# Kernel optimization log

Measured on AMD Instinct MI355X. Metric: run time of the kernel, lower is better.

## Reference

```python
import jax, jax.numpy as jnp
import numpy as np

B, D_IN, D_OUT, H, DEPTH = 16384, 512, 64, 256, 3
LR, ITERS, EPS = 0.1, 50, 1e-5


def setup_inputs() -> dict:
    key = jax.random.key(0)
    ks = jax.random.split(key, 8)
    d = {}
    d["x"] = jax.random.normal(ks[0], (B, D_IN), jnp.float32)
    d["y0"] = jax.random.normal(ks[1], (B, D_OUT), jnp.float32)
    cur = D_IN + D_OUT
    for i in range(DEPTH):
        d[f"W{i}"] = jax.random.normal(ks[2 + i], (H, cur), jnp.float32) / np.sqrt(cur).astype(np.float32)
        d[f"b{i}"] = jnp.zeros((H,), jnp.float32)
        d[f"g{i}"] = jnp.ones((H,), jnp.float32)
        d[f"be{i}"] = jnp.zeros((H,), jnp.float32)
        cur = H
    d["Wout"] = jax.random.normal(ks[5], (1, H), jnp.float32) / np.sqrt(H).astype(np.float32)
    d["bout"] = jnp.zeros((1,), jnp.float32)
    return d


def _energy(x, y, layers, out_layer):
    # E(x, y): concat -> [Linear -> LayerNorm -> SiLU] * depth -> Linear(1)
    h = jnp.concatenate([x, y], axis=-1)  # [B, D_IN+D_OUT]
    for (W, b, g, be) in layers:
        h = h @ W.T + b  # [B, H]
        mu = jnp.mean(h, axis=-1, keepdims=True)
        var = jnp.var(h, axis=-1, keepdims=True)  # biased, matching torch LayerNorm
        h = (h - mu) * jax.lax.rsqrt(var + EPS) * g + be
        h = h * jax.nn.sigmoid(h)  # SiLU
    Wout, bout = out_layer
    return h @ Wout.T + bout  # [B, 1]


def reference(x, y0, W0, b0, g0, be0, W1, b1, g1, be1, W2, b2, g2, be2, Wout, bout):
    layers = [(W0, b0, g0, be0), (W1, b1, g1, be1), (W2, b2, g2, be2)]
    out_layer = (Wout, bout)

    def e_mean(y):
        return jnp.mean(_energy(x, y, layers, out_layer))

    def step(y, _):
        # SGD on y: y <- y - lr * grad_y E_mean
        return y - LR * jax.grad(e_mean)(y), None

    y_final, _ = jax.lax.scan(step, y0, None, length=ITERS)
    return y_final
```

## Files before the change

### kernel.cpp

```cpp
#include <hip/hip_runtime.h>


typedef unsigned short u16;
typedef u16 u16x4 __attribute__((ext_vector_type(4)));
typedef u16 u16x8 __attribute__((ext_vector_type(8)));
typedef float f32x4 __attribute__((ext_vector_type(4)));
typedef int i32x4 __attribute__((ext_vector_type(4)));
typedef __bf16 bf16x8 __attribute__((ext_vector_type(8)));

#define ITERS 50
#define EPSF 1e-5f
static constexpr float SCALE = 0.1f / 16384.0f;

#define OFF_W0X   0
#define OFF_W0Y   262144
#define OFF_W0YT  278528
#define OFF_W1    294912
#define OFF_W1T   360448
#define OFF_W2    425984
#define OFF_W2T   491520
#define OFF_WSC   557056

__device__ __forceinline__ float bf2f(u16 h) {
  union { unsigned int u; float f; } v; v.u = ((unsigned int)h) << 16; return v.f;
}
__device__ __forceinline__ u16 f2bf(float f) {
  union { float f; unsigned int u; } v; v.f = f;
  unsigned int u = v.u;
  return (u16)((u + 0x7FFFu + ((u >> 16) & 1u)) >> 16);
}
__device__ __forceinline__ f32x4 mfma16(u16x8 a, u16x8 b, f32x4 c) {
  return __builtin_amdgcn_mfma_f32_16x16x32_bf16(
      __builtin_bit_cast(bf16x8, a), __builtin_bit_cast(bf16x8, b), c, 0, 0, 0);
}
__device__ __forceinline__ i32x4 mfma8(i32x4 a, i32x4 b, i32x4 c) {
  return __builtin_amdgcn_mfma_i32_16x16x64_i8(a, b, c, 0, 0, 0);
}
__device__ __forceinline__ int qpack4(const float* v, float qs) {
  int r = 0;
#pragma unroll
  for (int e = 0; e < 4; ++e) {
    float c = fmaxf(-127.f, fminf(127.f, v[e] * qs));
    int xi = __float2int_rn(c);
    r |= (xi & 255) << (8 * e);
  }
  return r;
}

__global__ void prep_w0x(const float* __restrict__ W0, u16* __restrict__ dst) {
  int i = blockIdx.x * 256 + threadIdx.x;
  if (i < 131072) dst[i] = f2bf(W0[(i >> 9) * 576 + (i & 511)]);
}

__global__ void prep_quant(const float* __restrict__ W0, const float* __restrict__ W1,
                           const float* __restrict__ W2, char* __restrict__ ws) {
  int wid = blockIdx.x * 4 + (threadIdx.x >> 6);
  int lane = threadIdx.x & 63;
  float* sc = (float*)(ws + OFF_WSC);
  if (wid < 256) {
    float v = W0[wid * 576 + 512 + lane];
    float mx = fabsf(v);
#pragma unroll
    for (int m = 1; m < 64; m <<= 1) mx = fmaxf(mx, __shfl_xor(mx, m));
    float qs = mx > 0.f ? 127.f / mx : 0.f;
    float c = fmaxf(-127.f, fminf(127.f, v * qs));
    ws[OFF_W0Y + wid * 64 + lane] = (char)__float2int_rn(c);
    if (lane == 0) sc[wid] = mx * (1.f / 127.f);
    return;
  }
  float v[4];
  char* dst;
  if (wid < 320) {
    int r = wid - 256;
#pragma unroll
    for (int e = 0; e < 4; ++e) v[e] = W0[(4 * lane + e) * 576 + 512 + r];
    dst = ws + OFF_W0YT + r * 256;
  } else if (wid < 576) {
    int r = wid - 320;
#pragma unroll
    for (int e = 0; e < 4; ++e) v[e] = W1[r * 256 + 4 * lane + e];
    dst = ws + OFF_W1 + r * 256;
  } else if (wid < 832) {
    int r = wid - 576;
#pragma unroll
    for (int e = 0; e < 4; ++e) v[e] = W1[(4 * lane + e) * 256 + r];
    dst = ws + OFF_W1T + r * 256;
  } else if (wid < 1088) {
    int r = wid - 832;
#pragma unroll
    for (int e = 0; e < 4; ++e) v[e] = W2[r * 256 + 4 * lane + e];
    dst = ws + OFF_W2 + r * 256;
  } else {
    int r = wid - 1088;
#pragma unroll
    for (int e = 0; e < 4; ++e) v[e] = W2[(4 * lane + e) * 256 + r];
    dst = ws + OFF_W2T + r * 256;
  }
  float mx = fmaxf(fmaxf(fabsf(v[0]), fabsf(v[1])), fmaxf(fabsf(v[2]), fabsf(v[3])));
#pragma unroll
  for (int m = 1; m < 64; m <<= 1) mx = fmaxf(mx, __shfl_xor(mx, m));
  float qs = mx > 0.f ? 127.f / mx : 0.f;
  ((int*)dst)[lane] = qpack4(v, qs);
  if (lane == 0) sc[wid] = mx * (1.f / 127.f);
}

template <int KS, int LDB, int AST>
__device__ __forceinline__ void gemm8(const char* A, const char* __restrict__ Bg,
                                      i32x4 (&acc)[2][4], int w, int l15, int q) {
  const char* Ab = A + l15 * AST + q * 16;
  const char* Bb = Bg + (64 * w + l15) * LDB + q * 16;
#pragma unroll
  for (int ks = 0; ks < KS; ++ks) {
    i32x4 b[4];
#pragma unroll
    for (int j = 0; j < 4; ++j) b[j] = *(const i32x4*)(Bb + 16 * j * LDB + ks * 64);
#pragma unroll
    for (int i = 0; i < 2; ++i) {
      i32x4 a = *(const i32x4*)(Ab + 16 * i * AST + ks * 64);
#pragma unroll
      for (int j = 0; j < 4; ++j) acc[i][j] = mfma8(a, b[j], acc[i][j]);
    }
  }
}

__device__ __forceinline__ void gemm_dy8(const char* A, const char* __restrict__ BT,
                                         i32x4 (&dy)[2], int mi, int nb, int l15, int q) {
  const char* Ab = A + (mi * 16 + l15) * 272 + q * 16;
  const char* B0 = BT + (nb + l15) * 256 + q * 16;
  const char* B1 = BT + (nb + 16 + l15) * 256 + q * 16;
#pragma unroll
  for (int ks = 0; ks < 4; ++ks) {
    i32x4 a = *(const i32x4*)(Ab + ks * 64);
    dy[0] = mfma8(a, *(const i32x4*)(B0 + ks * 64), dy[0]);
    dy[1] = mfma8(a, *(const i32x4*)(B1 + ks * 64), dy[1]);
  }
}

__device__ __forceinline__ void epi8(u16* gdst, const i32x4 (&acc)[2][4],
                                     const float* sRow, const float* sCol,
                                     int w, int l15, int q) {
#pragma unroll
  for (int i = 0; i < 2; ++i)
#pragma unroll
    for (int j = 0; j < 4; ++j) {
      int col = 64 * w + 16 * j + l15;
      float sc = sCol[col];
#pragma unroll
      for (int rr = 0; rr < 4; ++rr) {
        int row = 16 * i + 4 * q + rr;
        gdst[row * 264 + col] = f2bf((float)acc[i][j][rr] * sRow[row] * sc);
      }
    }
}

__device__ __forceinline__ void ew_fwd8(const u16* gIn, char* zqOut, float* szh,
                                        char* aOut, float* sAo, const float* bias,
                                        const float* g, const float* be,
                                        float* invOut, int t) {
  const int r = t >> 3, cg = t & 7;
  const u16* zp = gIn + r * 264 + 4 * cg;
  float z[32];
#pragma unroll
  for (int u = 0; u < 8; ++u) {
    u16x4 v = *(const u16x4*)(zp + 32 * u);
#pragma unroll
    for (int e = 0; e < 4; ++e) z[4 * u + e] = bf2f(v[e]);
  }
  if (bias) {
#pragma unroll
    for (int u = 0; u < 8; ++u) {
      f32x4 bv = *(const f32x4*)(bias + 32 * u + 4 * cg);
#pragma unroll
      for (int e = 0; e < 4; ++e) z[4 * u + e] += bv[e];
    }
  }
  float s = 0.f, ss = 0.f;
#pragma unroll
  for (int k = 0; k < 32; ++k) { s += z[k]; ss += z[k] * z[k]; }
  s += __shfl_xor(s, 1); ss += __shfl_xor(ss, 1);
  s += __shfl_xor(s, 2); ss += __shfl_xor(ss, 2);
  s += __shfl_xor(s, 4); ss += __shfl_xor(ss, 4);
  const float mu = s * (1.f / 256.f);
  const float var = ss * (1.f / 256.f) - mu * mu;
  const float inv = rsqrtf(var + EPSF);
  if (cg == 0) invOut[r] = inv;
  float a[32];
  float mzh = 0.f, ma = 0.f;
#pragma unroll
  for (int u = 0; u < 8; ++u) {
    f32x4 gv = *(const f32x4*)(g + 32 * u + 4 * cg);
    f32x4 bev = *(const f32x4*)(be + 32 * u + 4 * cg);
#pragma unroll
    for (int e = 0; e < 4; ++e) {
      const int k = 4 * u + e;
      float zn = (z[k] - mu) * inv;
      z[k] = zn;
      mzh = fmaxf(mzh, fabsf(zn));
      float uu = zn * gv[e] + bev[e];
      float av = uu / (1.f + __expf(-uu));
      a[k] = av;
      ma = fmaxf(ma, fabsf(av));
    }
  }
  mzh = fmaxf(mzh, __shfl_xor(mzh, 1)); ma = fmaxf(ma, __shfl_xor(ma, 1));
  mzh = fmaxf(mzh, __shfl_xor(mzh, 2)); ma = fmaxf(ma, __shfl_xor(ma, 2));
  mzh = fmaxf(mzh, __shfl_xor(mzh, 4)); ma = fmaxf(ma, __shfl_xor(ma, 4));
  float qz = mzh > 0.f ? 127.f / mzh : 0.f;
  float qa = ma > 0.f ? 127.f / ma : 0.f;
  if (cg == 0) { szh[r] = mzh * (1.f / 127.f); sAo[r] = ma * (1.f / 127.f); }
#pragma unroll
  for (int u = 0; u < 8; ++u) {
    *(int*)(zqOut + r * 272 + 32 * u + 4 * cg) = qpack4(&z[4 * u], qz);
    *(int*)(aOut + r * 272 + 32 * u + 4 * cg) = qpack4(&a[4 * u], qa);
  }
}

__device__ __forceinline__ void ew_l2_8(const u16* gIn, char* dOut, float* sAo,
                                        const float* bias, const float* g,
                                        const float* be, const float* wo, int t) {
  const int r = t >> 3, cg = t & 7;
  const u16* zp = gIn + r * 264 + 4 * cg;
  float zh[32], dzh[32];
  float s = 0.f, ss = 0.f;
#pragma unroll
  for (int u = 0; u < 8; ++u) {
    u16x4 v = *(const u16x4*)(zp + 32 * u);
    f32x4 bv = *(const f32x4*)(bias + 32 * u + 4 * cg);
#pragma unroll
    for (int e = 0; e < 4; ++e) {
      float zz = bf2f(v[e]) + bv[e];
      zh[4 * u + e] = zz; s += zz; ss += zz * zz;
    }
  }
  s += __shfl_xor(s, 1); ss += __shfl_xor(ss, 1);
  s += __shfl_xor(s, 2); ss += __shfl_xor(ss, 2);
  s += __shfl_xor(s, 4); ss += __shfl_xor(ss, 4);
  const float mu = s * (1.f / 256.f);
  const float var = ss * (1.f / 256.f) - mu * mu;
  const float inv = rsqrtf(var + EPSF);
  float s1 = 0.f, s2 = 0.f;
#pragma unroll
  for (int u = 0; u < 8; ++u) {
    f32x4 gv = *(const f32x4*)(g + 32 * u + 4 * cg);
    f32x4 bev = *(const f32x4*)(be + 32 * u + 4 * cg);
    f32x4 wv = *(const f32x4*)(wo + 32 * u + 4 * cg);
#pragma unroll
    for (int e = 0; e < 4; ++e) {
      const int k = 4 * u + e;
      float zn = (zh[k] - mu) * inv;
      zh[k] = zn;
      float uu = zn * gv[e] + bev[e];
      float sg = 1.f / (1.f + __expf(-uu));
      float du = wv[e] * sg * (1.f + uu * (1.f - sg));
      float d = du * gv[e];
      dzh[k] = d; s1 += d; s2 += d * zn;
    }
  }
  s1 += __shfl_xor(s1, 1); s2 += __shfl_xor(s2, 1);
  s1 += __shfl_xor(s1, 2); s2 += __shfl_xor(s2, 2);
  s1 += __shfl_xor(s1, 4); s2 += __shfl_xor(s2, 4);
  const float m1 = s1 * (1.f / 256.f), m2 = s2 * (1.f / 256.f);
  float mx = 0.f;
#pragma unroll
  for (int k = 0; k < 32; ++k) {
    dzh[k] = inv * (dzh[k] - m1 - zh[k] * m2);
    mx = fmaxf(mx, fabsf(dzh[k]));
  }
  mx = fmaxf(mx, __shfl_xor(mx, 1));
  mx = fmaxf(mx, __shfl_xor(mx, 2));
  mx = fmaxf(mx, __shfl_xor(mx, 4));
  float qd = mx > 0.f ? 127.f / mx : 0.f;
  if (cg == 0) sAo[r] = mx * (1.f / 127.f);
#pragma unroll
  for (int u = 0; u < 8; ++u)
    *(int*)(dOut + r * 272 + 32 * u + 4 * cg) = qpack4(&dzh[4 * u], qd);
}

__device__ __forceinline__ void ew_bwd8(const u16* gIn, const char* zq, const float* szh,
                                        const float* invArr, const float* g,
                                        const float* be, char* dOut, float* sAo, int t) {
  const int r = t >> 3, cg = t & 7;
  const u16* dp = gIn + r * 264 + 4 * cg;
  const char* zp = zq + r * 272 + 4 * cg;
  const float inv = invArr[r];
  const float szr = szh[r];
  float zh[32], dzh[32];
  float s1 = 0.f, s2 = 0.f;
#pragma unroll
  for (int u = 0; u < 8; ++u) {
    u16x4 dv = *(const u16x4*)(dp + 32 * u);
    int zi = *(const int*)(zp + 32 * u);
    f32x4 gv = *(const f32x4*)(g + 32 * u + 4 * cg);
    f32x4 bev = *(const f32x4*)(be + 32 * u + 4 * cg);
#pragma unroll
    for (int e = 0; e < 4; ++e) {
      const int k = 4 * u + e;
      float zn = (float)((signed char)(zi >> (8 * e))) * szr;
      float da = bf2f(dv[e]);
      float uu = zn * gv[e] + bev[e];
      float sg = 1.f / (1.f + __expf(-uu));
      float du = da * sg * (1.f + uu * (1.f - sg));
      float d = du * gv[e];
      zh[k] = zn; dzh[k] = d; s1 += d; s2 += d * zn;
    }
  }
  s1 += __shfl_xor(s1, 1); s2 += __shfl_xor(s2, 1);
  s1 += __shfl_xor(s1, 2); s2 += __shfl_xor(s2, 2);
  s1 += __shfl_xor(s1, 4); s2 += __shfl_xor(s2, 4);
  const float m1 = s1 * (1.f / 256.f), m2 = s2 * (1.f / 256.f);
  float mx = 0.f;
#pragma unroll
  for (int k = 0; k < 32; ++k) {
    dzh[k] = inv * (dzh[k] - m1 - zh[k] * m2);
    mx = fmaxf(mx, fabsf(dzh[k]));
  }
  mx = fmaxf(mx, __shfl_xor(mx, 1));
  mx = fmaxf(mx, __shfl_xor(mx, 2));
  mx = fmaxf(mx, __shfl_xor(mx, 4));
  float qd = mx > 0.f ? 127.f / mx : 0.f;
  if (cg == 0) sAo[r] = mx * (1.f / 127.f);
#pragma unroll
  for (int u = 0; u < 8; ++u)
    *(int*)(dOut + r * 272 + 32 * u + 4 * cg) = qpack4(&dzh[4 * u], qd);
}

__global__ __launch_bounds__(256, 2) void descent_kernel(
    const float* __restrict__ x, const float* __restrict__ y0,
    const float* __restrict__ b0, const float* __restrict__ g0, const float* __restrict__ be0,
    const float* __restrict__ b1, const float* __restrict__ g1, const float* __restrict__ be1,
    const float* __restrict__ b2, const float* __restrict__ g2, const float* __restrict__ be2,
    const float* __restrict__ wout, const char* __restrict__ ws, float* __restrict__ out) {
  __shared__ __align__(16) char zq0[32 * 272];
  __shared__ __align__(16) char zq1[32 * 272];
  __shared__ __align__(16) char A8[32 * 272];
  __shared__ __align__(16) u16 gT[32 * 264];
  __shared__ __align__(16) char yb[32 * 80];
  __shared__ float params[9 * 256];
  __shared__ float wsc[1344];
  __shared__ float sA[32], szh0[32], szh1[32], sY[32];
  __shared__ float invs[2][32];
  __shared__ float smax[4 * 16];

  const int t = threadIdx.x;
  const int w = t >> 6, lane = t & 63, l15 = lane & 15, q = lane >> 4;
  const int rowbase = blockIdx.x * 32;

  const u16* W0X = (const u16*)(ws + OFF_W0X);
  const char* W0Yq = ws + OFF_W0Y;
  const char* W0YTq = ws + OFF_W0YT;
  const char* W1q = ws + OFF_W1;
  const char* W1Tq = ws + OFF_W1T;
  const char* W2q = ws + OFF_W2;
  const char* W2Tq = ws + OFF_W2T;
  const float* wscg = (const float*)(ws + OFF_WSC);

  params[0 * 256 + t] = g0[t];  params[1 * 256 + t] = be0[t];
  params[2 * 256 + t] = g1[t];  params[3 * 256 + t] = be1[t];
  params[4 * 256 + t] = g2[t];  params[5 * 256 + t] = be2[t];
  params[6 * 256 + t] = b1[t];  params[7 * 256 + t] = b2[t];
  params[8 * 256 + t] = wout[t];
#pragma unroll
  for (int k = 0; k < 6; ++k) {
    int idx = t + 256 * k;
    if (idx < 1344) wsc[idx] = wscg[idx];
  }

  const int mi = w >> 1, nb = (w & 1) * 32;
  float yv[2][4];
#pragma unroll
  for (int j = 0; j < 2; ++j)
#pragma unroll
    for (int rr = 0; rr < 4; ++rr)
      yv[j][rr] = y0[(rowbase + mi * 16 + q * 4 + rr) * 64 + nb + 16 * j + l15];

  const f32x4 z4 = {0.f, 0.f, 0.f, 0.f};

  f32x4 cR[2][4];
#pragma unroll
  for (int i = 0; i < 2; ++i)
#pragma unroll
    for (int j = 0; j < 4; ++j) cR[i][j] = z4;
  {
    const float* xp0 = x + (rowbase + l15) * 512 + q * 8;
    const u16* Bb = W0X + (64 * w + l15) * 512 + q * 8;
#pragma unroll 4
    for (int ks = 0; ks < 16; ++ks) {
      u16x8 b[4];
#pragma unroll
      for (int j = 0; j < 4; ++j) b[j] = *(const u16x8*)(Bb + 16 * j * 512 + ks * 32);
#pragma unroll
      for (int i = 0; i < 2; ++i) {
        const float* xp = xp0 + i * 16 * 512 + ks * 32;
        f32x4 x0 = *(const f32x4*)xp;
        f32x4 x1 = *(const f32x4*)(xp + 4);
        u16x8 a;
#pragma unroll
        for (int e = 0; e < 4; ++e) { a[e] = f2bf(x0[e]); a[4 + e] = f2bf(x1[e]); }
#pragma unroll
        for (int j = 0; j < 4; ++j) cR[i][j] = mfma16(a, b[j], cR[i][j]);
      }
    }
#pragma unroll
    for (int j = 0; j < 4; ++j) {
      float bb = b0[64 * w + 16 * j + l15];
#pragma unroll
      for (int i = 0; i < 2; ++i)
#pragma unroll
        for (int rr = 0; rr < 4; ++rr) cR[i][j][rr] += bb;
    }
  }
  __syncthreads();

  for (int it = 0; it < ITERS; ++it) {
    float mx[4];
#pragma unroll
    for (int rr = 0; rr < 4; ++rr)
      mx[rr] = fmaxf(fabsf(yv[0][rr]), fabsf(yv[1][rr]));
#pragma unroll
    for (int m = 1; m < 16; m <<= 1)
#pragma unroll
      for (int rr = 0; rr < 4; ++rr) mx[rr] = fmaxf(mx[rr], __shfl_xor(mx[rr], m));
    if (l15 == 0)
#pragma unroll
      for (int rr = 0; rr < 4; ++rr) smax[w * 16 + q * 4 + rr] = mx[rr];
    __syncthreads();
#pragma unroll
    for (int rr = 0; rr < 4; ++rr) {
      float m2 = fmaxf(mx[rr], smax[(w ^ 1) * 16 + q * 4 + rr]);
      float qy = m2 > 0.f ? 127.f / m2 : 0.f;
      int row = 16 * mi + 4 * q + rr;
      if (l15 == 0 && (w & 1) == 0) sY[row] = m2 * (1.f / 127.f);
#pragma unroll
      for (int j = 0; j < 2; ++j) {
        float c = fmaxf(-127.f, fminf(127.f, yv[j][rr] * qy));
        yb[row * 80 + nb + 16 * j + l15] = (char)__float2int_rn(c);
      }
    }
    __syncthreads();

    i32x4 acc[2][4];
#pragma unroll
    for (int i = 0; i < 2; ++i)
#pragma unroll
      for (int j = 0; j < 4; ++j) acc[i][j] = (i32x4){0, 0, 0, 0};
    gemm8<1, 64, 80>(yb, W0Yq, acc, w, l15, q);
#pragma unroll
    for (int i = 0; i < 2; ++i)
#pragma unroll
      for (int j = 0; j < 4; ++j) {
        int col = 64 * w + 16 * j + l15;
        float sc = wsc[col];
#pragma unroll
        for (int rr = 0; rr < 4; ++rr) {
          int row = 16 * i + 4 * q + rr;
          gT[row * 264 + col] = f2bf(cR[i][j][rr] + (float)acc[i][j][rr] * sY[row] * sc);
        }
      }
    __syncthreads();
    ew_fwd8(gT, zq0, szh0, A8, sA, nullptr, &params[0 * 256], &params[1 * 256],
            invs[0], t);
    __syncthreads();

#pragma unroll
    for (int i = 0; i < 2; ++i)
#pragma unroll
      for (int j = 0; j < 4; ++j) acc[i][j] = (i32x4){0, 0, 0, 0};
    gemm8<4, 256, 272>(A8, W1q, acc, w, l15, q);
    epi8(gT, acc, sA, &wsc[320], w, l15, q);
    __syncthreads();
    ew_fwd8(gT, zq1, szh1, A8, sA, &params[6 * 256], &params[2 * 256],
            &params[3 * 256], invs[1], t);
    __syncthreads();

#pragma unroll
    for (int i = 0; i < 2; ++i)
#pragma unroll
      for (int j = 0; j < 4; ++j) acc[i][j] = (i32x4){0, 0, 0, 0};
    gemm8<4, 256, 272>(A8, W2q, acc, w, l15, q);
    epi8(gT, acc, sA, &wsc[832], w, l15, q);
    __syncthreads();
    ew_l2_8(gT, A8, sA, &params[7 * 256], &params[4 * 256], &params[5 * 256],
            &params[8 * 256], t);
    __syncthreads();

#pragma unroll
    for (int i = 0; i < 2; ++i)
#pragma unroll
      for (int j = 0; j < 4; ++j) acc[i][j] = (i32x4){0, 0, 0, 0};
    gemm8<4, 256, 272>(A8, W2Tq, acc, w, l15, q);
    epi8(gT, acc, sA, &wsc[1088], w, l15, q);
    __syncthreads();
    ew_bwd8(gT, zq1, szh1, invs[1], &params[2 * 256], &params[3 * 256], A8, sA, t);
    __syncthreads();

#pragma unroll
    for (int i = 0; i < 2; ++i)
#pragma unroll
      for (int j = 0; j < 4; ++j) acc[i][j] = (i32x4){0, 0, 0, 0};
    gemm8<4, 256, 272>(A8, W1Tq, acc, w, l15, q);
    epi8(gT, acc, sA, &wsc[576], w, l15, q);
    __syncthreads();
    ew_bwd8(gT, zq0, szh0, invs[0], &params[0 * 256], &params[1 * 256], A8, sA, t);
    __syncthreads();

    i32x4 dy[2] = {{0, 0, 0, 0}, {0, 0, 0, 0}};
    gemm_dy8(A8, W0YTq, dy, mi, nb, l15, q);
#pragma unroll
    for (int j = 0; j < 2; ++j)
#pragma unroll
      for (int rr = 0; rr < 4; ++rr) {
        int row = 16 * mi + 4 * q + rr;
        yv[j][rr] -= SCALE * (float)dy[j][rr] * sA[row] * wsc[256 + nb + 16 * j + l15];
      }
  }

#pragma unroll
  for (int j = 0; j < 2; ++j)
#pragma unroll
    for (int rr = 0; rr < 4; ++rr)
      out[(rowbase + mi * 16 + q * 4 + rr) * 64 + nb + 16 * j + l15] = yv[j][rr];
}

extern "C" void kernel_launch(void* const* d_in, const int* in_sizes, int n_in,
                              void* d_out, int out_size, void* d_ws, size_t ws_size,
                              hipStream_t stream) {
  const float* x   = (const float*)d_in[0];
  const float* y0  = (const float*)d_in[1];
  const float* W0  = (const float*)d_in[2];
  const float* b0  = (const float*)d_in[3];
  const float* g0  = (const float*)d_in[4];
  const float* be0 = (const float*)d_in[5];
  const float* W1  = (const float*)d_in[6];
  const float* b1  = (const float*)d_in[7];
  const float* g1  = (const float*)d_in[8];
  const float* be1 = (const float*)d_in[9];
  const float* W2  = (const float*)d_in[10];
  const float* b2  = (const float*)d_in[11];
  const float* g2  = (const float*)d_in[12];
  const float* be2 = (const float*)d_in[13];
  const float* wout = (const float*)d_in[14];
  char* ws = (char*)d_ws;
  float* out = (float*)d_out;

  prep_w0x<<<512, 256, 0, stream>>>(W0, (u16*)(ws + OFF_W0X));
  prep_quant<<<336, 256, 0, stream>>>(W0, W1, W2, ws);
  descent_kernel<<<512, 256, 0, stream>>>(x, y0, b0, g0, be0, b1, g1, be1,
                                          b2, g2, be2, wout, ws, out);
}
```

Measured before the change: 2.308 ms.

## Cut shared memory and registers to raise occupancy in int8 descent kernel

Replaces per-row weight quantization scales with per-tensor scales computed by a new absmax kernel. It keeps the saved normalized activations and the LayerNorm inverse-std in registers as packed bf16 instead of int8 shared buffers. It also shrinks the staging buffer, packs the layer-0 residual into bf16 pairs, and raises launch bounds from 2 to 4 blocks per SM. Smaller pieces: truncating bf16 conversion, rcp-based sigmoid, perm-based int8 packing, and bias folded into the GEMM epilogue. The aim is higher occupancy and less shared-memory traffic, at the cost of coarser weight quantization and possible register pressure or spills.

```diff
diff --git a/kernel.cpp b/kernel.cpp
--- a/kernel.cpp
+++ b/kernel.cpp
@@ -2,6 +2,7 @@
 
 
 typedef unsigned short u16;
+typedef u16 u16x2 __attribute__((ext_vector_type(2)));
 typedef u16 u16x4 __attribute__((ext_vector_type(4)));
 typedef u16 u16x8 __attribute__((ext_vector_type(8)));
 typedef float f32x4 __attribute__((ext_vector_type(4)));
@@ -10,6 +11,8 @@
 
 #define ITERS 50
 #define EPSF 1e-5f
+#define STG 262
+#define AST 272
 static constexpr float SCALE = 0.1f / 16384.0f;
 
 #define OFF_W0X   0
@@ -24,10 +27,30 @@
 __device__ __forceinline__ float bf2f(u16 h) {
   union { unsigned int u; float f; } v; v.u = ((unsigned int)h) << 16; return v.f;
 }
+__device__ __forceinline__ u16 f2bt(float f) {
+  return (u16)(__builtin_bit_cast(unsigned int, f) >> 16);
+}
 __device__ __forceinline__ u16 f2bf(float f) {
-  union { float f; unsigned int u; } v; v.f = f;
-  unsigned int u = v.u;
+  unsigned int u = __builtin_bit_cast(unsigned int, f);
   return (u16)((u + 0x7FFFu + ((u >> 16) & 1u)) >> 16);
+}
+__device__ __forceinline__ float uplo(int p) {
+  return __builtin_bit_cast(float, (unsigned int)p << 16);
+}
+__device__ __forceinline__ float uphi(int p) {
+  return __builtin_bit_cast(float, (unsigned int)p & 0xffff0000u);
+}
+__device__ __forceinline__ int packbf2(float lo, float hi) {
+  return __builtin_amdgcn_perm(__builtin_bit_cast(int, hi),
+                               __builtin_bit_cast(int, lo), 0x07060302);
+}
+__device__ __forceinline__ int pack_i8x4(float a0, float a1, float a2, float a3,
+                                         float qs) {
+  int b0 = __float2int_rn(a0 * qs), b1 = __float2int_rn(a1 * qs);
+  int b2 = __float2int_rn(a2 * qs), b3 = __float2int_rn(a3 * qs);
+  int t01 = __builtin_amdgcn_perm(b1, b0, 0x00000400);
+  int t23 = __builtin_amdgcn_perm(b3, b2, 0x00000400);
+  return __builtin_amdgcn_perm(t23, t01, 0x05040100);
 }
 __device__ __forceinline__ f32x4 mfma16(u16x8 a, u16x8 b, f32x4 c) {
   return __builtin_amdgcn_mfma_f32_16x16x32_bf16(
@@ -36,78 +59,72 @@
 __device__ __forceinline__ i32x4 mfma8(i32x4 a, i32x4 b, i32x4 c) {
   return __builtin_amdgcn_mfma_i32_16x16x64_i8(a, b, c, 0, 0, 0);
 }
-__device__ __forceinline__ int qpack4(const float* v, float qs) {
-  int r = 0;
-#pragma unroll
-  for (int e = 0; e < 4; ++e) {
-    float c = fmaxf(-127.f, fminf(127.f, v[e] * qs));
-    int xi = __float2int_rn(c);
-    r |= (xi & 255) << (8 * e);
-  }
-  return r;
-}
 
 __global__ void prep_w0x(const float* __restrict__ W0, u16* __restrict__ dst) {
   int i = blockIdx.x * 256 + threadIdx.x;
   if (i < 131072) dst[i] = f2bf(W0[(i >> 9) * 576 + (i & 511)]);
 }
 
+__global__ void prep_init(float* sc) { if (threadIdx.x < 8) sc[threadIdx.x] = 0.f; }
+
+__global__ void prep_absmax(const float* __restrict__ W0, const float* __restrict__ W1,
+                            const float* __restrict__ W2, float* sc) {
+  int i = blockIdx.x * 256 + threadIdx.x;
+  float v; int slot;
+  if (i < 16384)       { v = fabsf(W0[(i >> 6) * 576 + 512 + (i & 63)]); slot = 0; }
+  else if (i < 81920)  { v = fabsf(W1[i - 16384]); slot = 1; }
+  else                 { v = fabsf(W2[i - 81920]); slot = 2; }
+#pragma unroll
+  for (int m = 1; m < 64; m <<= 1) v = fmaxf(v, __shfl_xor(v, m));
+  if ((threadIdx.x & 63) == 0)
+    atomicMax((unsigned int*)(sc + slot), __builtin_bit_cast(unsigned int, v));
+}
+
 __global__ void prep_quant(const float* __restrict__ W0, const float* __restrict__ W1,
                            const float* __restrict__ W2, char* __restrict__ ws) {
+  const float* sc = (const float*)(ws + OFF_WSC);
   int wid = blockIdx.x * 4 + (threadIdx.x >> 6);
   int lane = threadIdx.x & 63;
-  float* sc = (float*)(ws + OFF_WSC);
   if (wid < 256) {
+    float qs = sc[0] > 0.f ? 127.f / sc[0] : 0.f;
     float v = W0[wid * 576 + 512 + lane];
-    float mx = fabsf(v);
-#pragma unroll
-    for (int m = 1; m < 64; m <<= 1) mx = fmaxf(mx, __shfl_xor(mx, m));
-    float qs = mx > 0.f ? 127.f / mx : 0.f;
-    float c = fmaxf(-127.f, fminf(127.f, v * qs));
-    ws[OFF_W0Y + wid * 64 + lane] = (char)__float2int_rn(c);
-    if (lane == 0) sc[wid] = mx * (1.f / 127.f);
+    ws[OFF_W0Y + wid * 64 + lane] = (char)__float2int_rn(v * qs);
     return;
   }
-  float v[4];
-  char* dst;
+  float v[4]; char* dst; float qs;
   if (wid < 320) {
-    int r = wid - 256;
+    int r = wid - 256; qs = sc[0] > 0.f ? 127.f / sc[0] : 0.f;
 #pragma unroll
     for (int e = 0; e < 4; ++e) v[e] = W0[(4 * lane + e) * 576 + 512 + r];
     dst = ws + OFF_W0YT + r * 256;
   } else if (wid < 576) {
-    int r = wid - 320;
+    int r = wid - 320; qs = sc[1] > 0.f ? 127.f / sc[1] : 0.f;
 #pragma unroll
     for (int e = 0; e < 4; ++e) v[e] = W1[r * 256 + 4 * lane + e];
     dst = ws + OFF_W1 + r * 256;
   } else if (wid < 832) {
-    int r = wid - 576;
+    int r = wid - 576; qs = sc[1] > 0.f ? 127.f / sc[1] : 0.f;
 #pragma unroll
     for (int e = 0; e < 4; ++e) v[e] = W1[(4 * lane + e) * 256 + r];
     dst = ws + OFF_W1T + r * 256;
   } else if (wid < 1088) {
-    int r = wid - 832;
+    int r = wid - 832; qs = sc[2] > 0.f ? 127.f / sc[2] : 0.f;
 #pragma unroll
     for (int e = 0; e < 4; ++e) v[e] = W2[r * 256 + 4 * lane + e];
     dst = ws + OFF_W2 + r * 256;
   } else {
-    int r = wid - 1088;
+    int r = wid - 1088; qs = sc[2] > 0.f ? 127.f / sc[2] : 0.f;
 #pragma unroll
     for (int e = 0; e < 4; ++e) v[e] = W2[(4 * lane + e) * 256 + r];
     dst = ws + OFF_W2T + r * 256;
   }
-  float mx = fmaxf(fmaxf(fabsf(v[0]), fabsf(v[1])), fmaxf(fabsf(v[2]), fabsf(v[3])));
-#pragma unroll
-  for (int m = 1; m < 64; m <<= 1) mx = fmaxf(mx, __shfl_xor(mx, m));
-  float qs = mx > 0.f ? 127.f / mx : 0.f;
-  ((int*)dst)[lane] = qpack4(v, qs);
-  if (lane == 0) sc[wid] = mx * (1.f / 127.f);
-}
-
-template <int KS, int LDB, int AST>
+  ((int*)dst)[lane] = pack_i8x4(v[0], v[1], v[2], v[3], qs);
+}
+
+template <int KS, int LDB, int ASTt>
 __device__ __forceinline__ void gemm8(const char* A, const char* __restrict__ Bg,
                                       i32x4 (&acc)[2][4], int w, int l15, int q) {
-  const char* Ab = A + l15 * AST + q * 16;
+  const char* Ab = A + l15 * ASTt + q * 16;
   const char* Bb = Bg + (64 * w + l15) * LDB + q * 16;
 #pragma unroll
   for (int ks = 0; ks < KS; ++ks) {
@@ -116,7 +133,7 @@
     for (int j = 0; j < 4; ++j) b[j] = *(const i32x4*)(Bb + 16 * j * LDB + ks * 64);
 #pragma unroll
     for (int i = 0; i < 2; ++i) {
-      i32x4 a = *(const i32x4*)(Ab + 16 * i * AST + ks * 64);
+      i32x4 a = *(const i32x4*)(Ab + 16 * i * ASTt + ks * 64);
 #pragma unroll
       for (int j = 0; j < 4; ++j) acc[i][j] = mfma8(a, b[j], acc[i][j]);
     }
@@ -125,7 +142,7 @@
 
 __device__ __forceinline__ void gemm_dy8(const char* A, const char* __restrict__ BT,
                                          i32x4 (&dy)[2], int mi, int nb, int l15, int q) {
-  const char* Ab = A + (mi * 16 + l15) * 272 + q * 16;
+  const char* Ab = A + (mi * 16 + l15) * AST + q * 16;
   const char* B0 = BT + (nb + l15) * 256 + q * 16;
   const char* B1 = BT + (nb + 16 + l15) * 256 + q * 16;
 #pragma unroll
@@ -136,101 +153,97 @@
   }
 }
 
-__device__ __forceinline__ void epi8(u16* gdst, const i32x4 (&acc)[2][4],
-                                     const float* sRow, const float* sCol,
-                                     int w, int l15, int q) {
-#pragma unroll
-  for (int i = 0; i < 2; ++i)
+__device__ __forceinline__ void epi_stage(u16* stg, const i32x4 (&acc)[2][4],
+                                          const float* rowsc, float sW,
+                                          const float* bias, int w, int l15, int q) {
+#pragma unroll
+  for (int i = 0; i < 2; ++i) {
+    float rs[4];
+#pragma unroll
+    for (int rr = 0; rr < 4; ++rr) rs[rr] = rowsc[16 * i + 4 * q + rr] * sW;
 #pragma unroll
     for (int j = 0; j < 4; ++j) {
       int col = 64 * w + 16 * j + l15;
-      float sc = sCol[col];
-#pragma unroll
-      for (int rr = 0; rr < 4; ++rr) {
-        int row = 16 * i + 4 * q + rr;
-        gdst[row * 264 + col] = f2bf((float)acc[i][j][rr] * sRow[row] * sc);
-      }
-    }
-}
-
-__device__ __forceinline__ void ew_fwd8(const u16* gIn, char* zqOut, float* szh,
-                                        char* aOut, float* sAo, const float* bias,
-                                        const float* g, const float* be,
-                                        float* invOut, int t) {
+      float b = bias ? bias[col] : 0.f;
+#pragma unroll
+      for (int rr = 0; rr < 4; ++rr)
+        stg[(16 * i + 4 * q + rr) * STG + col] =
+            f2bt((float)acc[i][j][rr] * rs[rr] + b);
+    }
+  }
+}
+
+__device__ __forceinline__ float ew_fwd(const u16* stg_, const float* g,
+                                        const float* be, int* zq, char* A8_,
+                                        float* sAArr, int t) {
   const int r = t >> 3, cg = t & 7;
-  const u16* zp = gIn + r * 264 + 4 * cg;
+  const u16* zp = stg_ + r * STG;
   float z[32];
 #pragma unroll
-  for (int u = 0; u < 8; ++u) {
-    u16x4 v = *(const u16x4*)(zp + 32 * u);
-#pragma unroll
-    for (int e = 0; e < 4; ++e) z[4 * u + e] = bf2f(v[e]);
-  }
-  if (bias) {
-#pragma unroll
-    for (int u = 0; u < 8; ++u) {
-      f32x4 bv = *(const f32x4*)(bias + 32 * u + 4 * cg);
-#pragma unroll
-      for (int e = 0; e < 4; ++e) z[4 * u + e] += bv[e];
-    }
+  for (int k = 0; k < 8; ++k) {
+    int c0 = 32 * k + 4 * cg;
+    u16x2 va = *(const u16x2*)(zp + c0);
+    u16x2 vb = *(const u16x2*)(zp + c0 + 2);
+    z[4 * k] = bf2f(va[0]); z[4 * k + 1] = bf2f(va[1]);
+    z[4 * k + 2] = bf2f(vb[0]); z[4 * k + 3] = bf2f(vb[1]);
   }
   float s = 0.f, ss = 0.f;
 #pragma unroll
-  for (int k = 0; k < 32; ++k) { s += z[k]; ss += z[k] * z[k]; }
+  for (int m = 0; m < 32; ++m) { s += z[m]; ss += z[m] * z[m]; }
   s += __shfl_xor(s, 1); ss += __shfl_xor(ss, 1);
   s += __shfl_xor(s, 2); ss += __shfl_xor(ss, 2);
   s += __shfl_xor(s, 4); ss += __shfl_xor(ss, 4);
   const float mu = s * (1.f / 256.f);
   const float var = ss * (1.f / 256.f) - mu * mu;
   const float inv = rsqrtf(var + EPSF);
-  if (cg == 0) invOut[r] = inv;
-  float a[32];
-  float mzh = 0.f, ma = 0.f;
-#pragma unroll
-  for (int u = 0; u < 8; ++u) {
-    f32x4 gv = *(const f32x4*)(g + 32 * u + 4 * cg);
-    f32x4 bev = *(const f32x4*)(be + 32 * u + 4 * cg);
+  float ma = 0.f;
+#pragma unroll
+  for (int k = 0; k < 8; ++k) {
+    int c0 = 32 * k + 4 * cg;
+    f32x4 gv = *(const f32x4*)(g + c0);
+    f32x4 bv = *(const f32x4*)(be + c0);
+    float zn[4];
+#pragma unroll
+    for (int e = 0; e < 4; ++e) zn[e] = (z[4 * k + e] - mu) * inv;
+    zq[2 * k] = packbf2(zn[0], zn[1]);
+    zq[2 * k + 1] = packbf2(zn[2], zn[3]);
 #pragma unroll
     for (int e = 0; e < 4; ++e) {
-      const int k = 4 * u + e;
-      float zn = (z[k] - mu) * inv;
-      z[k] = zn;
-      mzh = fmaxf(mzh, fabsf(zn));
-      float uu = zn * gv[e] + bev[e];
-      float av = uu / (1.f + __expf(-uu));
-      a[k] = av;
+      float uu = zn[e] * gv[e] + bv[e];
+      float av = uu * __builtin_amdgcn_rcpf(1.f + __expf(-uu));
+      z[4 * k + e] = av;
       ma = fmaxf(ma, fabsf(av));
     }
   }
-  mzh = fmaxf(mzh, __shfl_xor(mzh, 1)); ma = fmaxf(ma, __shfl_xor(ma, 1));
-  mzh = fmaxf(mzh, __shfl_xor(mzh, 2)); ma = fmaxf(ma, __shfl_xor(ma, 2));
-  mzh = fmaxf(mzh, __shfl_xor(mzh, 4)); ma = fmaxf(ma, __shfl_xor(ma, 4));
-  float qz = mzh > 0.f ? 127.f / mzh : 0.f;
+  ma = fmaxf(ma, __shfl_xor(ma, 1));
+  ma = fmaxf(ma, __shfl_xor(ma, 2));
+  ma = fmaxf(ma, __shfl_xor(ma, 4));
   float qa = ma > 0.f ? 127.f / ma : 0.f;
-  if (cg == 0) { szh[r] = mzh * (1.f / 127.f); sAo[r] = ma * (1.f / 127.f); }
-#pragma unroll
-  for (int u = 0; u < 8; ++u) {
-    *(int*)(zqOut + r * 272 + 32 * u + 4 * cg) = qpack4(&z[4 * u], qz);
-    *(int*)(aOut + r * 272 + 32 * u + 4 * cg) = qpack4(&a[4 * u], qa);
-  }
-}
-
-__device__ __forceinline__ void ew_l2_8(const u16* gIn, char* dOut, float* sAo,
-                                        const float* bias, const float* g,
-                                        const float* be, const float* wo, int t) {
+  if (cg == 0) sAArr[r] = ma * (1.f / 127.f);
+  char* ap = A8_ + r * AST;
+#pragma unroll
+  for (int k = 0; k < 8; ++k)
+    *(int*)(ap + 32 * k + 4 * cg) =
+        pack_i8x4(z[4 * k], z[4 * k + 1], z[4 * k + 2], z[4 * k + 3], qa);
+  return inv;
+}
+
+__device__ __forceinline__ void ew_l2(const u16* stg_, const float* g,
+                                      const float* be, const float* wo, char* A8_,
+                                      float* sAArr, int t) {
   const int r = t >> 3, cg = t & 7;
-  const u16* zp = gIn + r * 264 + 4 * cg;
-  float zh[32], dzh[32];
+  const u16* zp = stg_ + r * STG;
+  float z[32];
   float s = 0.f, ss = 0.f;
 #pragma unroll
-  for (int u = 0; u < 8; ++u) {
-    u16x4 v = *(const u16x4*)(zp + 32 * u);
-    f32x4 bv = *(const f32x4*)(bias + 32 * u + 4 * cg);
-#pragma unroll
-    for (int e = 0; e < 4; ++e) {
-      float zz = bf2f(v[e]) + bv[e];
-      zh[4 * u + e] = zz; s += zz; ss += zz * zz;
-    }
+  for (int k = 0; k < 8; ++k) {
+    int c0 = 32 * k + 4 * cg;
+    u16x2 va = *(const u16x2*)(zp + c0);
+    u16x2 vb = *(const u16x2*)(zp + c0 + 2);
+    z[4 * k] = bf2f(va[0]); z[4 * k + 1] = bf2f(va[1]);
+    z[4 * k + 2] = bf2f(vb[0]); z[4 * k + 3] = bf2f(vb[1]);
+#pragma unroll
+    for (int e = 0; e < 4; ++e) { float v = z[4 * k + e]; s += v; ss += v * v; }
   }
   s += __shfl_xor(s, 1); ss += __shfl_xor(ss, 1);
   s += __shfl_xor(s, 2); ss += __shfl_xor(ss, 2);
@@ -240,20 +253,20 @@
   const float inv = rsqrtf(var + EPSF);
   float s1 = 0.f, s2 = 0.f;
 #pragma unroll
-  for (int u = 0; u < 8; ++u) {
-    f32x4 gv = *(const f32x4*)(g + 32 * u + 4 * cg);
-    f32x4 bev = *(const f32x4*)(be + 32 * u + 4 * cg);
-    f32x4 wv = *(const f32x4*)(wo + 32 * u + 4 * cg);
+  for (int k = 0; k < 8; ++k) {
+    int c0 = 32 * k + 4 * cg;
+    f32x4 gv = *(const f32x4*)(g + c0);
+    f32x4 bv = *(const f32x4*)(be + c0);
+    f32x4 wv = *(const f32x4*)(wo + c0);
 #pragma unroll
     for (int e = 0; e < 4; ++e) {
-      const int k = 4 * u + e;
-      float zn = (zh[k] - mu) * inv;
-      zh[k] = zn;
-      float uu = zn * gv[e] + bev[e];
-      float sg = 1.f / (1.f + __expf(-uu));
+      float zn = (z[4 * k + e] - mu) * inv;
+      z[4 * k + e] = zn;
+      float uu = zn * gv[e] + bv[e];
+      float sg = __builtin_amdgcn_rcpf(1.f + __expf(-uu));
       float du = wv[e] * sg * (1.f + uu * (1.f - sg));
       float d = du * gv[e];
-      dzh[k] = d; s1 += d; s2 += d * zn;
+      s1 += d; s2 += d * zn;
     }
   }
   s1 += __shfl_xor(s1, 1); s2 += __shfl_xor(s2, 1);
@@ -262,46 +275,57 @@
   const float m1 = s1 * (1.f / 256.f), m2 = s2 * (1.f / 256.f);
   float mx = 0.f;
 #pragma unroll
-  for (int k = 0; k < 32; ++k) {
-    dzh[k] = inv * (dzh[k] - m1 - zh[k] * m2);
-    mx = fmaxf(mx, fabsf(dzh[k]));
+  for (int k = 0; k < 8; ++k) {
+    int c0 = 32 * k + 4 * cg;
+    f32x4 gv = *(const f32x4*)(g + c0);
+    f32x4 bv = *(const f32x4*)(be + c0);
+    f32x4 wv = *(const f32x4*)(wo + c0);
+#pragma unroll
+    for (int e = 0; e < 4; ++e) {
+      float zn = z[4 * k + e];
+      float uu = zn * gv[e] + bv[e];
+      float sg = __builtin_amdgcn_rcpf(1.f + __expf(-uu));
+      float du = wv[e] * sg * (1.f + uu * (1.f - sg));
+      float dz = inv * (du * gv[e] - m1 - zn * m2);
+      z[4 * k + e] = dz;
+      mx = fmaxf(mx, fabsf(dz));
+    }
   }
   mx = fmaxf(mx, __shfl_xor(mx, 1));
   mx = fmaxf(mx, __shfl_xor(mx, 2));
   mx = fmaxf(mx, __shfl_xor(mx, 4));
   float qd = mx > 0.f ? 127.f / mx : 0.f;
-  if (cg == 0) sAo[r] = mx * (1.f / 127.f);
-#pragma unroll
-  for (int u = 0; u < 8; ++u)
-    *(int*)(dOut + r * 272 + 32 * u + 4 * cg) = qpack4(&dzh[4 * u], qd);
-}
-
-__device__ __forceinline__ void ew_bwd8(const u16* gIn, const char* zq, const float* szh,
-                                        const float* invArr, const float* g,
-                                        const float* be, char* dOut, float* sAo, int t) {
+  if (cg == 0) sAArr[r] = mx * (1.f / 127.f);
+  char* ap = A8_ + r * AST;
+#pragma unroll
+  for (int k = 0; k < 8; ++k)
+    *(int*)(ap + 32 * k + 4 * cg) =
+        pack_i8x4(z[4 * k], z[4 * k + 1], z[4 * k + 2], z[4 * k + 3], qd);
+}
+
+__device__ __forceinline__ void ew_bwd(const u16* stg_, const int* zq, float inv,
+                                       const float* g, const float* be, char* A8_,
+                                       float* sAArr, int t) {
   const int r = t >> 3, cg = t & 7;
-  const u16* dp = gIn + r * 264 + 4 * cg;
-  const char* zp = zq + r * 272 + 4 * cg;
-  const float inv = invArr[r];
-  const float szr = szh[r];
-  float zh[32], dzh[32];
+  const u16* dp = stg_ + r * STG;
+  float d_[32];
   float s1 = 0.f, s2 = 0.f;
 #pragma unroll
-  for (int u = 0; u < 8; ++u) {
-    u16x4 dv = *(const u16x4*)(dp + 32 * u);
-    int zi = *(const int*)(zp + 32 * u);
-    f32x4 gv = *(const f32x4*)(g + 32 * u + 4 * cg);
-    f32x4 bev = *(const f32x4*)(be + 32 * u + 4 * cg);
+  for (int k = 0; k < 8; ++k) {
+    int c0 = 32 * k + 4 * cg;
+    u16x2 va = *(const u16x2*)(dp + c0);
+    u16x2 vb = *(const u16x2*)(dp + c0 + 2);
+    float da[4] = {bf2f(va[0]), bf2f(va[1]), bf2f(vb[0]), bf2f(vb[1])};
+    f32x4 gv = *(const f32x4*)(g + c0);
+    f32x4 bv = *(const f32x4*)(be + c0);
 #pragma unroll
     for (int e = 0; e < 4; ++e) {
-      const int k = 4 * u + e;
-      float zn = (float)((signed char)(zi >> (8 * e))) * szr;
-      float da = bf2f(dv[e]);
-      float uu = zn * gv[e] + bev[e];
-      float sg = 1.f / (1.f + __expf(-uu));
-      float du = da * sg * (1.f + uu * (1.f - sg));
-      float d = du * gv[e];
-      zh[k] = zn; dzh[k] = d; s1 += d; s2 += d * zn;
+      float zn = (e & 1) ? uphi(zq[2 * k + (e >> 1)]) : uplo(zq[2 * k + (e >> 1)]);
+      float uu = zn * gv[e] + bv[e];
+      float sg = __builtin_amdgcn_rcpf(1.f + __expf(-uu));
+      float du = da[e] * sg * (1.f + uu * (1.f - sg));
+      float dd = du * gv[e];
+      d_[4 * k + e] = dd; s1 += dd; s2 += dd * zn;
     }
   }
   s1 += __shfl_xor(s1, 1); s2 += __shfl_xor(s2, 1);
@@ -310,36 +334,36 @@
   const float m1 = s1 * (1.f / 256.f), m2 = s2 * (1.f / 256.f);
   float mx = 0.f;
 #pragma unroll
-  for (int k = 0; k < 32; ++k) {
-    dzh[k] = inv * (dzh[k] - m1 - zh[k] * m2);
-    mx = fmaxf(mx, fabsf(dzh[k]));
+  for (int m = 0; m < 32; ++m) {
+    float zn = (m & 1) ? uphi(zq[m >> 1]) : uplo(zq[m >> 1]);
+    float dz = inv * (d_[m] - m1 - zn * m2);
+    d_[m] = dz;
+    mx = fmaxf(mx, fabsf(dz));
   }
   mx = fmaxf(mx, __shfl_xor(mx, 1));
   mx = fmaxf(mx, __shfl_xor(mx, 2));
   mx = fmaxf(mx, __shfl_xor(mx, 4));
   float qd = mx > 0.f ? 127.f / mx : 0.f;
-  if (cg == 0) sAo[r] = mx * (1.f / 127.f);
-#pragma unroll
-  for (int u = 0; u < 8; ++u)
-    *(int*)(dOut + r * 272 + 32 * u + 4 * cg) = qpack4(&dzh[4 * u], qd);
-}
-
-__global__ __launch_bounds__(256, 2) void descent_kernel(
+  if (cg == 0) sAArr[r] = mx * (1.f / 127.f);
+  char* ap = A8_ + r * AST;
+#pragma unroll
+  for (int k = 0; k < 8; ++k)
+    *(int*)(ap + 32 * k + 4 * cg) =
+        pack_i8x4(d_[4 * k], d_[4 * k + 1], d_[4 * k + 2], d_[4 * k + 3], qd);
+}
+
+__global__ __launch_bounds__(256, 4) void descent_kernel(
     const float* __restrict__ x, const float* __restrict__ y0,
     const float* __restrict__ b0, const float* __restrict__ g0, const float* __restrict__ be0,
     const float* __restrict__ b1, const float* __restrict__ g1, const float* __restrict__ be1,
     const float* __restrict__ b2, const float* __restrict__ g2, const float* __restrict__ be2,
     const float* __restrict__ wout, const char* __restrict__ ws, float* __restrict__ out) {
-  __shared__ __align__(16) char zq0[32 * 272];
-  __shared__ __align__(16) char zq1[32 * 272];
-  __shared__ __align__(16) char A8[32 * 272];
-  __shared__ __align__(16) u16 gT[32 * 264];
+  __shared__ __align__(16) u16 stg[32 * STG];
+  __shared__ __align__(16) char A8[32 * AST];
   __shared__ __align__(16) char yb[32 * 80];
-  __shared__ float params[9 * 256];
-  __shared__ float wsc[1344];
-  __shared__ float sA[32], szh0[32], szh1[32], sY[32];
-  __shared__ float invs[2][32];
-  __shared__ float smax[4 * 16];
+  __shared__ __align__(16) float params[9 * 256];
+  __shared__ float sA[32], sY[32];
+  __shared__ float smax[64];
 
   const int t = threadIdx.x;
   const int w = t >> 6, lane = t & 63, l15 = lane & 15, q = lane >> 4;
@@ -352,18 +376,16 @@
   const char* W1Tq = ws + OFF_W1T;
   const char* W2q = ws + OFF_W2;
   const char* W2Tq = ws + OFF_W2T;
-  const float* wscg = (const float*)(ws + OFF_WSC);
+  const float* scg = (const float*)(ws + OFF_WSC);
+  const float sW0Yd = scg[0] * (1.f / 127.f);
+  const float sW1d = scg[1] * (1.f / 127.f);
+  const float sW2d = scg[2] * (1.f / 127.f);
 
   params[0 * 256 + t] = g0[t];  params[1 * 256 + t] = be0[t];
   params[2 * 256 + t] = g1[t];  params[3 * 256 + t] = be1[t];
   params[4 * 256 + t] = g2[t];  params[5 * 256 + t] = be2[t];
   params[6 * 256 + t] = b1[t];  params[7 * 256 + t] = b2[t];
   params[8 * 256 + t] = wout[t];
-#pragma unroll
-  for (int k = 0; k < 6; ++k) {
-    int idx = t + 256 * k;
-    if (idx < 1344) wsc[idx] = wscg[idx];
-  }
 
   const int mi = w >> 1, nb = (w & 1) * 32;
   float yv[2][4];
@@ -375,12 +397,13 @@
 
   const f32x4 z4 = {0.f, 0.f, 0.f, 0.f};
 
-  f32x4 cR[2][4];
-#pragma unroll
-  for (int i = 0; i < 2; ++i)
-#pragma unroll
-    for (int j = 0; j < 4; ++j) cR[i][j] = z4;
+  int cRp[2][4][2];
   {
+    f32x4 cR[2][4];
+#pragma unroll
+    for (int i = 0; i < 2; ++i)
+#pragma unroll
+      for (int j = 0; j < 4; ++j) cR[i][j] = z4;
     const float* xp0 = x + (rowbase + l15) * 512 + q * 8;
     const u16* Bb = W0X + (64 * w + l15) * 512 + q * 8;
 #pragma unroll 4
@@ -404,12 +427,18 @@
     for (int j = 0; j < 4; ++j) {
       float bb = b0[64 * w + 16 * j + l15];
 #pragma unroll
-      for (int i = 0; i < 2; ++i)
+      for (int i = 0; i < 2; ++i) {
 #pragma unroll
         for (int rr = 0; rr < 4; ++rr) cR[i][j][rr] += bb;
+        cRp[i][j][0] = packbf2(cR[i][j][0], cR[i][j][1]);
+        cRp[i][j][1] = packbf2(cR[i][j][2], cR[i][j][3]);
+      }
     }
   }
   __syncthreads();
+
+  int zq0[16], zq1[16];
+  float inv0 = 0.f, inv1 = 0.f;
 
   for (int it = 0; it < ITERS; ++it) {
     float mx[4];
@@ -431,10 +460,8 @@
       int row = 16 * mi + 4 * q + rr;
       if (l15 == 0 && (w & 1) == 0) sY[row] = m2 * (1.f / 127.f);
 #pragma unroll
-      for (int j = 0; j < 2; ++j) {
-        float c = fmaxf(-127.f, fminf(127.f, yv[j][rr] * qy));
-        yb[row * 80 + nb + 16 * j + l15] = (char)__float2int_rn(c);
-      }
+      for (int j = 0; j < 2; ++j)
+        yb[row * 80 + nb + 16 * j + l15] = (char)__float2int_rn(yv[j][rr] * qy);
     }
     __syncthreads();
 
@@ -445,73 +472,76 @@
       for (int j = 0; j < 4; ++j) acc[i][j] = (i32x4){0, 0, 0, 0};
     gemm8<1, 64, 80>(yb, W0Yq, acc, w, l15, q);
 #pragma unroll
-    for (int i = 0; i < 2; ++i)
+    for (int i = 0; i < 2; ++i) {
+      float rs[4];
+#pragma unroll
+      for (int rr = 0; rr < 4; ++rr) rs[rr] = sY[16 * i + 4 * q + rr] * sW0Yd;
 #pragma unroll
       for (int j = 0; j < 4; ++j) {
         int col = 64 * w + 16 * j + l15;
-        float sc = wsc[col];
-#pragma unroll
-        for (int rr = 0; rr < 4; ++rr) {
-          int row = 16 * i + 4 * q + rr;
-          gT[row * 264 + col] = f2bf(cR[i][j][rr] + (float)acc[i][j][rr] * sY[row] * sc);
+#pragma unroll
+        for (int p = 0; p < 2; ++p) {
+          float ce = uplo(cRp[i][j][p]), co = uphi(cRp[i][j][p]);
+          stg[(16 * i + 4 * q + 2 * p) * STG + col] =
+              f2bt(ce + (float)acc[i][j][2 * p] * rs[2 * p]);
+          stg[(16 * i + 4 * q + 2 * p + 1) * STG + col] =
+              f2bt(co + (float)acc[i][j][2 * p + 1] * rs[2 * p + 1]);
         }
       }
-    __syncthreads();
-    ew_fwd8(gT, zq0, szh0, A8, sA, nullptr, &params[0 * 256], &params[1 * 256],
-            invs[0], t);
+    }
+    __syncthreads();
+    inv0 = ew_fwd(stg, &params[0 * 256], &params[1 * 256], zq0, A8, sA, t);
     __syncthreads();
 
 #pragma unroll
     for (int i = 0; i < 2; ++i)
 #pragma unroll
       for (int j = 0; j < 4; ++j) acc[i][j] = (i32x4){0, 0, 0, 0};
-    gemm8<4, 256, 272>(A8, W1q, acc, w, l15, q);
-    epi8(gT, acc, sA, &wsc[320], w, l15, q);
-    __syncthreads();
-    ew_fwd8(gT, zq1, szh1, A8, sA, &params[6 * 256], &params[2 * 256],
-            &params[3 * 256], invs[1], t);
+    gemm8<4, 256, AST>(A8, W1q, acc, w, l15, q);
+    epi_stage(stg, acc, sA, sW1d, &params[6 * 256], w, l15, q);
+    __syncthreads();
+    inv1 = ew_fwd(stg, &params[2 * 256], &params[3 * 256], zq1, A8, sA, t);
     __syncthreads();
 
 #pragma unroll
     for (int i = 0; i < 2; ++i)
 #pragma unroll
       for (int j = 0; j < 4; ++j) acc[i][j] = (i32x4){0, 0, 0, 0};
-    gemm8<4, 256, 272>(A8, W2q, acc, w, l15, q);
-    epi8(gT, acc, sA, &wsc[832], w, l15, q);
-    __syncthreads();
-    ew_l2_8(gT, A8, sA, &params[7 * 256], &params[4 * 256], &params[5 * 256],
-            &params[8 * 256], t);
+    gemm8<4, 256, AST>(A8, W2q, acc, w, l15, q);
+    epi_stage(stg, acc, sA, sW2d, &params[7 * 256], w, l15, q);
+    __syncthreads();
+    ew_l2(stg, &params[4 * 256], &params[5 * 256], &params[8 * 256], A8, sA, t);
     __syncthreads();
 
 #pragma unroll
     for (int i = 0; i < 2; ++i)
 #pragma unroll
       for (int j = 0; j < 4; ++j) acc[i][j] = (i32x4){0, 0, 0, 0};
-    gemm8<4, 256, 272>(A8, W2Tq, acc, w, l15, q);
-    epi8(gT, acc, sA, &wsc[1088], w, l15, q);
-    __syncthreads();
-    ew_bwd8(gT, zq1, szh1, invs[1], &params[2 * 256], &params[3 * 256], A8, sA, t);
+    gemm8<4, 256, AST>(A8, W2Tq, acc, w, l15, q);
+    epi_stage(stg, acc, sA, sW2d, nullptr, w, l15, q);
+    __syncthreads();
+    ew_bwd(stg, zq1, inv1, &params[2 * 256], &params[3 * 256], A8, sA, t);
     __syncthreads();
 
 #pragma unroll
     for (int i = 0; i < 2; ++i)
 #pragma unroll
       for (int j = 0; j < 4; ++j) acc[i][j] = (i32x4){0, 0, 0, 0};
-    gemm8<4, 256, 272>(A8, W1Tq, acc, w, l15, q);
-    epi8(gT, acc, sA, &wsc[576], w, l15, q);
-    __syncthreads();
-    ew_bwd8(gT, zq0, szh0, invs[0], &params[0 * 256], &params[1 * 256], A8, sA, t);
+    gemm8<4, 256, AST>(A8, W1Tq, acc, w, l15, q);
+    epi_stage(stg, acc, sA, sW1d, nullptr, w, l15, q);
+    __syncthreads();
+    ew_bwd(stg, zq0, inv0, &params[0 * 256], &params[1 * 256], A8, sA, t);
     __syncthreads();
 
     i32x4 dy[2] = {{0, 0, 0, 0}, {0, 0, 0, 0}};
     gemm_dy8(A8, W0YTq, dy, mi, nb, l15, q);
-#pragma unroll
-    for (int j = 0; j < 2; ++j)
-#pragma unroll
-      for (int rr = 0; rr < 4; ++rr) {
-        int row = 16 * mi + 4 * q + rr;
-        yv[j][rr] -= SCALE * (float)dy[j][rr] * sA[row] * wsc[256 + nb + 16 * j + l15];
-      }
+    const float dsc = SCALE * sW0Yd;
+#pragma unroll
+    for (int rr = 0; rr < 4; ++rr) {
+      float rsc = sA[16 * mi + 4 * q + rr] * dsc;
+#pragma unroll
+      for (int j = 0; j < 2; ++j) yv[j][rr] -= (float)dy[j][rr] * rsc;
+    }
   }
 
 #pragma unroll
@@ -543,6 +573,8 @@
   float* out = (float*)d_out;
 
   prep_w0x<<<512, 256, 0, stream>>>(W0, (u16*)(ws + OFF_W0X));
+  prep_init<<<1, 64, 0, stream>>>((float*)(ws + OFF_WSC));
+  prep_absmax<<<576, 256, 0, stream>>>(W0, W1, W2, (float*)(ws + OFF_WSC));
   prep_quant<<<336, 256, 0, stream>>>(W0, W1, W2, ws);
   descent_kernel<<<512, 256, 0, stream>>>(x, y0, b0, g0, be0, b1, g1, be1,
                                           b2, g2, be2, wout, ws, out);
```

Measured after the change: 2.976 ms. 29.0% more time.
